# Optimization experiments

Measured on AMD Instinct MI355X. Metric: run time of the kernel, lower is better.

The kernel has to match this reference:

```python
import jax, jax.numpy as jnp
import numpy as np

OBS_LEN = 20
K = 20          # number of latent samples (leading dim of pred_lstm_hidden)
B = 4096        # batch
C = 2           # n_coordinates
H = 128         # z_dim + s_dim
MH = 64         # mapping hidden dim


def hardsigmoid(x):
    return jnp.clip(x / 6.0 + 0.5, 0.0, 1.0)


def hardtanh(x):
    return jnp.clip(x, -1.0, 1.0)


def setup_inputs() -> dict:
    key = jax.random.key(0)
    ks = jax.random.split(key, 12)
    std = 0.1  # _initialize_weights: normal(0, 0.1), biases zero
    return {
        "obs_traj_rel": jax.random.normal(ks[0], (OBS_LEN, B, C), jnp.float32),
        "pred_lstm_hidden": jax.random.normal(ks[1], (K, B, H), jnp.float32),
        # mapping MLP: Linear(H, MH) + LeakyReLU, Linear(MH, H)
        "Wm1": std * jax.random.normal(ks[2], (MH, H), jnp.float32),
        "bm1": jnp.zeros((MH,), jnp.float32),
        "Wm2": std * jax.random.normal(ks[3], (H, MH), jnp.float32),
        "bm2": jnp.zeros((H,), jnp.float32),
        # custom LSTMCell params
        "W_ih": std * jax.random.normal(ks[4], (4 * H, C), jnp.float32),
        "W_hh": std * jax.random.normal(ks[5], (4 * H, H), jnp.float32),
        "b_ih": jnp.zeros((4 * H,), jnp.float32),
        "b_hh": jnp.zeros((4 * H,), jnp.float32),
        # pred_hidden2pos: Linear(H, C)
        "W_out": std * jax.random.normal(ks[6], (C, H), jnp.float32),
        "b_out": jnp.zeros((C,), jnp.float32),
    }


def reference(obs_traj_rel, pred_lstm_hidden, Wm1, bm1, Wm2, bm2,
              W_ih, W_hh, b_ih, b_hh, W_out, b_out):
    # mapping MLP over last dim: [K, B, H]
    h = jax.nn.leaky_relu(jnp.einsum('kbh,mh->kbm', pred_lstm_hidden, Wm1) + bm1)
    h = jnp.einsum('kbm,hm->kbh', h, Wm2) + bm2
    c = jnp.zeros_like(h)

    # step i uses obs_traj_rel[max(i-1, 0)]
    idx = np.concatenate([[0], np.arange(OBS_LEN - 1)])
    inputs_seq = obs_traj_rel[idx, :, :C]  # [T, B, C]

    def step(carry, x_t):
        h, c = carry  # each [K, B, H]
        # input term is identical across the K samples -> compute once, broadcast
        gi = x_t @ W_ih.T + b_ih                      # [B, 4H]
        gh = jnp.einsum('kbh,gh->kbg', h, W_hh) + b_hh  # [K, B, 4H]
        gates = gi[None] + gh
        i_g, f_g, g_g, o_g = jnp.split(gates, 4, axis=-1)
        c_new = hardsigmoid(f_g) * c + hardsigmoid(i_g) * hardtanh(g_g)
        h_new = hardsigmoid(o_g) * hardtanh(c_new)
        out = jnp.einsum('kbh,ch->kbc', h_new, W_out) + b_out  # [K, B, C]
        return (h_new, c_new), out

    _, outs = jax.lax.scan(step, (h, c), inputs_seq)
    return outs  # [obs_len, K, B, C]
```

## Files before the change

kernel.cpp:

```cpp
#include <hip/hip_runtime.h>

#define NT 20
#define BT 4096
#define HD 128
#define RT 81920
#define RB 64

typedef _Float16 half8 __attribute__((ext_vector_type(8)));
typedef _Float16 half2v __attribute__((ext_vector_type(2)));
typedef float f32x4 __attribute__((ext_vector_type(4)));
typedef float f32x2 __attribute__((ext_vector_type(2)));
typedef unsigned u32x4 __attribute__((ext_vector_type(4)));

#if defined(__has_builtin)
#  if __has_builtin(__builtin_amdgcn_fdot2)
#    define HAVE_FDOT2 1
#  endif
#endif

__device__ __forceinline__ float clamp01(float x) {
  return fminf(fmaxf(x, 0.0f), 1.0f);
}
__device__ __forceinline__ float htanh(float x) {
  return fminf(fmaxf(x, -1.0f), 1.0f);
}

__device__ __forceinline__ float dot2(half2v a, half2v b, float c) {
#ifdef HAVE_FDOT2
  return __builtin_amdgcn_fdot2(a, b, c, false);
#else
  return fmaf((float)a[0], (float)b[0], fmaf((float)a[1], (float)b[1], c));
#endif
}

__device__ __forceinline__ half8 ldcvt8s(const float* __restrict__ p, float s) {
  f32x4 a = *(const f32x4*)p;
  f32x4 b = *(const f32x4*)(p + 4);
  half8 r;
  r[0] = (_Float16)(a[0] * s); r[1] = (_Float16)(a[1] * s);
  r[2] = (_Float16)(a[2] * s); r[3] = (_Float16)(a[3] * s);
  r[4] = (_Float16)(b[0] * s); r[5] = (_Float16)(b[1] * s);
  r[6] = (_Float16)(b[2] * s); r[7] = (_Float16)(b[3] * s);
  return r;
}
__device__ __forceinline__ half8 ldcvt8(const float* __restrict__ p) {
  return ldcvt8s(p, 1.0f);
}

__device__ __forceinline__ void lds_barrier() {
  __builtin_amdgcn_sched_barrier(0);
  asm volatile("s_waitcnt lgkmcnt(0)" ::: "memory");
  __builtin_amdgcn_s_barrier();
  __builtin_amdgcn_sched_barrier(0);
}

__global__ __launch_bounds__(512, 2) void decoder_kernel(
    const float* __restrict__ obs, const float* __restrict__ pred,
    const float* __restrict__ Wm1, const float* __restrict__ bm1,
    const float* __restrict__ Wm2, const float* __restrict__ bm2,
    const float* __restrict__ W_ih, const float* __restrict__ W_hh,
    const float* __restrict__ b_ih, const float* __restrict__ b_hh,
    const float* __restrict__ W_out, const float* __restrict__ b_out,
    float* __restrict__ outp)
{
  __shared__ __align__(16) char lds[38400];
  const int tid = threadIdx.x;
  const int w   = tid >> 6;
  const int l   = tid & 63;
  const int l15 = l & 15;
  const int lg  = l >> 4;
  const int wm  = w & 3;
  const int wc  = w >> 2;
  const int r0  = blockIdx.x * RB;
  const int b0  = r0 & (BT - 1);

  char* const buf0 = lds;
  char* const h1l  = lds + 16384;
  char* const obsl = lds + 32768;
  char* const wol  = lds + 37888;

  const f32x4 fzero = {0.f, 0.f, 0.f, 0.f};
  const float SCL = 1.0f / 6.0f;

  const int rdmask = (l15 & 7) << 4;
  const int arow  = l15 * 256;
  const int base0 = (16 * lg) ^ rdmask;
  const int wcol2 = 32 * w + 2 * l15;

  int wbase[4];
#pragma unroll
  for (int reg = 0; reg < 4; ++reg) {
    int rr = 4 * lg + reg;
    wbase[reg] = rr * 256 + (wcol2 ^ ((rr & 7) << 4));
  }

  if (tid < 256) ((_Float16*)wol)[tid] = (_Float16)W_out[tid];
  for (int i = tid; i < NT * RB; i += 512) {
    int t = i >> 6, row = i & 63;
    int tp = (t > 0) ? t - 1 : 0;
    f32x2 xv = *(const f32x2*)(obs + ((size_t)tp * BT + b0 + row) * 2);
    half2v hp; hp[0] = (_Float16)xv[0]; hp[1] = (_Float16)xv[1];
    *(unsigned*)(obsl + (size_t)i * 4) = __builtin_bit_cast(unsigned, hp);
  }

  {
    half8 a1[4], b1[2][4];
#pragma unroll
    for (int kt = 0; kt < 4; ++kt)
      a1[kt] = ldcvt8(pred + (size_t)(r0 + 16 * wm + l15) * HD + kt * 32 + lg * 8);
#pragma unroll
    for (int j = 0; j < 2; ++j)
#pragma unroll
      for (int kt = 0; kt < 4; ++kt)
        b1[j][kt] = ldcvt8(Wm1 + (l15 + 16 * (2 * wc + j)) * HD + kt * 32 + lg * 8);
    f32x4 acc1[2] = {fzero, fzero};
#pragma unroll
    for (int kt = 0; kt < 4; ++kt)
#pragma unroll
      for (int j = 0; j < 2; ++j)
        acc1[j] = __builtin_amdgcn_mfma_f32_16x16x32_f16(a1[kt], b1[j][kt], acc1[j], 0, 0, 0);
#pragma unroll
    for (int j = 0; j < 2; ++j) {
      int c = l15 + 16 * (2 * wc + j);
      float bb = bm1[c];
#pragma unroll
      for (int reg = 0; reg < 4; ++reg) {
        int row = 16 * wm + 4 * lg + reg;
        float v = acc1[j][reg] + bb;
        v = v >= 0.f ? v : 0.01f * v;
        *(_Float16*)(h1l + row * 128 + ((2 * c) ^ ((row & 7) << 4))) = (_Float16)v;
      }
    }
  }
  __syncthreads();
  {
    half8 a2[2], b2[4][2];
#pragma unroll
    for (int kt = 0; kt < 2; ++kt)
      a2[kt] = *(const half8*)(h1l + (16 * wm + l15) * 128 + ((64 * kt + 16 * lg) ^ rdmask));
#pragma unroll
    for (int j = 0; j < 4; ++j)
#pragma unroll
      for (int kt = 0; kt < 2; ++kt)
        b2[j][kt] = ldcvt8(Wm2 + (l15 + 16 * (4 * wc + j)) * 64 + kt * 32 + lg * 8);
    f32x4 acc2[4] = {fzero, fzero, fzero, fzero};
#pragma unroll
    for (int kt = 0; kt < 2; ++kt)
#pragma unroll
      for (int j = 0; j < 4; ++j)
        acc2[j] = __builtin_amdgcn_mfma_f32_16x16x32_f16(a2[kt], b2[j][kt], acc2[j], 0, 0, 0);
#pragma unroll
    for (int j = 0; j < 4; ++j) {
      int c = l15 + 16 * (4 * wc + j);
      float bb = bm2[c];
#pragma unroll
      for (int reg = 0; reg < 4; ++reg) {
        int row = 16 * wm + 4 * lg + reg;
        float v = acc2[j][reg] + bb;
        *(_Float16*)(buf0 + row * 256 + ((2 * c) ^ ((row & 7) << 4))) = (_Float16)v;
      }
    }
  }

  half8 bW[4][4];
  half8 bAug[4];
#pragma unroll
  for (int n = 0; n < 4; ++n) {
    const float s = (n == 2) ? 1.0f : SCL;
    int g = 128 * n + 16 * w + l15;
#pragma unroll
    for (int kt = 0; kt < 4; ++kt)
      bW[n][kt] = ldcvt8s(W_hh + (size_t)g * HD + kt * 32 + lg * 8, s);
    half2v t2;
    t2[0] = (_Float16)(W_ih[g * 2 + 0] * s);
    t2[1] = (_Float16)(W_ih[g * 2 + 1] * s);
    float bs = b_ih[g] + b_hh[g];
    half2v t3;
    t3[0] = (_Float16)((n == 2) ? bs : bs * SCL + 0.5f);
    t3[1] = (_Float16)0.0f;
    unsigned v0 = (lg == 0) ? __builtin_bit_cast(unsigned, t2) : 0u;
    unsigned v1 = (lg == 0) ? __builtin_bit_cast(unsigned, t3) : 0u;
    u32x4 bu = {v0, v1, 0u, 0u};
    bAug[n] = __builtin_bit_cast(half8, bu);
  }
  const float bo = wc ? b_out[1] : b_out[0];

  f32x4 cst[4] = {fzero, fzero, fzero, fzero};

  __syncthreads();

  half8 wfr[4];
#pragma unroll
  for (int kt = 0; kt < 4; ++kt)
    wfr[kt] = *(const half8*)(wol + wc * 256 + kt * 64 + lg * 16);

  for (int t = 0; t < NT; ++t) {
    char* const brd = lds + ((t & 1) << 14);
    char* const bwr = lds + (((t & 1) ^ 1) << 14);

    half8 A[2][5];

    {
      const int mm0 = (wm + 1) & 3;
#pragma unroll
      for (int kt = 0; kt < 4; ++kt)
        A[0][kt] = *(const half8*)(brd + mm0 * 4096 + arow + ((64 * kt) ^ base0));
      unsigned xv = *(const unsigned*)(obsl + ((t << 6) + (mm0 << 4) + l15) * 4);
      unsigned u0 = (lg == 0) ? xv : 0u;
      unsigned u1 = (lg == 0) ? 0x00003C00u : 0u;
      u32x4 xu = {u0, u1, 0u, 0u};
      A[0][4] = __builtin_bit_cast(half8, xu);
    }

#pragma unroll
    for (int j = 0; j < 4; ++j) {
      const int mm = (wm + 1 + j) & 3;
      const int cur = j & 1;

      if (j < 3) {
        const int mn = (wm + 2 + j) & 3;
#pragma unroll
        for (int kt = 0; kt < 4; ++kt)
          A[cur ^ 1][kt] = *(const half8*)(brd + mn * 4096 + arow + ((64 * kt) ^ base0));
        unsigned xv = *(const unsigned*)(obsl + ((t << 6) + (mn << 4) + l15) * 4);
        unsigned u0 = (lg == 0) ? xv : 0u;
        unsigned u1 = (lg == 0) ? 0x00003C00u : 0u;
        u32x4 xu = {u0, u1, 0u, 0u};
        A[cur ^ 1][4] = __builtin_bit_cast(half8, xu);
      }

      f32x4 acc[4] = {fzero, fzero, fzero, fzero};
      __builtin_amdgcn_s_setprio(1);
#pragma unroll
      for (int kt = 0; kt < 5; ++kt) {
#pragma unroll
        for (int n = 0; n < 4; ++n) {
          const half8 bfrag = (kt < 4) ? bW[n][kt] : bAug[n];
          acc[n] = __builtin_amdgcn_mfma_f32_16x16x32_f16(A[cur][kt], bfrag, acc[n], 0, 0, 0);
        }
      }
      __builtin_amdgcn_s_setprio(0);

      if (j == 3 && t > 0) {
        float p = 0.f;
#pragma unroll
        for (int kt = 0; kt < 4; ++kt) {
          const half8 a = A[cur][kt];
          const half8 wf = wfr[kt];
#pragma unroll
          for (int pp = 0; pp < 4; ++pp) {
            half2v ha; ha[0] = a[2 * pp]; ha[1] = a[2 * pp + 1];
            half2v wa; wa[0] = wf[2 * pp]; wa[1] = wf[2 * pp + 1];
            p = dot2(ha, wa, p);
          }
        }
        p += __shfl_xor(p, 16, 64); p += __shfl_xor(p, 32, 64);
        if (l < 16)
          outp[(size_t)(t - 1) * (RT * 2) + (size_t)(r0 + 16 * wm + l) * 2 + wc] = p + bo;
      }

      f32x4 cn4;
#pragma unroll
      for (int reg = 0; reg < 4; ++reg) {
        float i_ = clamp01(acc[0][reg]);
        float f_ = clamp01(acc[1][reg]);
        float g_ = htanh(acc[2][reg]);
        float o_ = clamp01(acc[3][reg]);
        float cn = fmaf(f_, cst[j][reg], i_ * g_);
        cn4[reg] = cn;
        float hn = o_ * htanh(cn);
        *(_Float16*)(bwr + mm * 4096 + wbase[reg]) = (_Float16)hn;
      }
      cst[j] = cn4;
    }
    lds_barrier();
  }

  {
    float p = 0.f;
#pragma unroll
    for (int kt = 0; kt < 4; ++kt) {
      half8 a = *(const half8*)(buf0 + wm * 4096 + arow + ((64 * kt) ^ base0));
      const half8 wf = wfr[kt];
#pragma unroll
      for (int pp = 0; pp < 4; ++pp) {
        half2v ha; ha[0] = a[2 * pp]; ha[1] = a[2 * pp + 1];
        half2v wa; wa[0] = wf[2 * pp]; wa[1] = wf[2 * pp + 1];
        p = dot2(ha, wa, p);
      }
    }
    p += __shfl_xor(p, 16, 64); p += __shfl_xor(p, 32, 64);
    if (l < 16)
      outp[(size_t)19 * (RT * 2) + (size_t)(r0 + 16 * wm + l) * 2 + wc] = p + bo;
  }
}

extern "C" void kernel_launch(void* const* d_in, const int* in_sizes, int n_in,
                              void* d_out, int out_size, void* d_ws, size_t ws_size,
                              hipStream_t stream) {
  const float* obs   = (const float*)d_in[0];
  const float* pred  = (const float*)d_in[1];
  const float* Wm1   = (const float*)d_in[2];
  const float* bm1   = (const float*)d_in[3];
  const float* Wm2   = (const float*)d_in[4];
  const float* bm2   = (const float*)d_in[5];
  const float* W_ih  = (const float*)d_in[6];
  const float* W_hh  = (const float*)d_in[7];
  const float* b_ih  = (const float*)d_in[8];
  const float* b_hh  = (const float*)d_in[9];
  const float* W_out = (const float*)d_in[10];
  const float* b_out = (const float*)d_in[11];

  decoder_kernel<<<RT / RB, 512, 0, stream>>>(
      obs, pred, Wm1, bm1, Wm2, bm2, W_ih, W_hh, b_ih, b_hh, W_out, b_out,
      (float*)d_out);
}
```

Baseline: 303.9 us.

## Process 128 rows per block, interleaving two independent row halves per wave

Result: slower. 318.6 us (+4.9%).

```diff
diff --git a/kernel.cpp b/kernel.cpp
--- a/kernel.cpp
+++ b/kernel.cpp
@@ -4,7 +4,7 @@
 #define BT 4096
 #define HD 128
 #define RT 81920
-#define RB 64
+#define RB 128
 
 typedef _Float16 half8 __attribute__((ext_vector_type(8)));
 typedef _Float16 half2v __attribute__((ext_vector_type(2)));
@@ -63,7 +63,7 @@
     const float* __restrict__ W_out, const float* __restrict__ b_out,
     float* __restrict__ outp)
 {
-  __shared__ __align__(16) char lds[38400];
+  __shared__ __align__(16) char lds[76288];
   const int tid = threadIdx.x;
   const int w   = tid >> 6;
   const int l   = tid & 63;
@@ -75,9 +75,9 @@
   const int b0  = r0 & (BT - 1);
 
   char* const buf0 = lds;
-  char* const h1l  = lds + 16384;
-  char* const obsl = lds + 32768;
-  char* const wol  = lds + 37888;
+  char* const h1l  = lds + 32768;
+  char* const obsl = lds + 65536;
+  char* const wol  = lds + 75776;
 
   const f32x4 fzero = {0.f, 0.f, 0.f, 0.f};
   const float SCL = 1.0f / 6.0f;
@@ -96,7 +96,7 @@
 
   if (tid < 256) ((_Float16*)wol)[tid] = (_Float16)W_out[tid];
   for (int i = tid; i < NT * RB; i += 512) {
-    int t = i >> 6, row = i & 63;
+    int t = i >> 7, row = i & 127;
     int tp = (t > 0) ? t - 1 : 0;
     f32x2 xv = *(const f32x2*)(obs + ((size_t)tp * BT + b0 + row) * 2);
     half2v hp; hp[0] = (_Float16)xv[0]; hp[1] = (_Float16)xv[1];
@@ -104,62 +104,80 @@
   }
 
   {
-    half8 a1[4], b1[2][4];
-#pragma unroll
-    for (int kt = 0; kt < 4; ++kt)
-      a1[kt] = ldcvt8(pred + (size_t)(r0 + 16 * wm + l15) * HD + kt * 32 + lg * 8);
+    half8 a1[2][4], b1[2][4];
+#pragma unroll
+    for (int h = 0; h < 2; ++h)
+#pragma unroll
+      for (int kt = 0; kt < 4; ++kt)
+        a1[h][kt] = ldcvt8(pred + (size_t)(r0 + 64 * h + 16 * wm + l15) * HD + kt * 32 + lg * 8);
 #pragma unroll
     for (int j = 0; j < 2; ++j)
 #pragma unroll
       for (int kt = 0; kt < 4; ++kt)
         b1[j][kt] = ldcvt8(Wm1 + (l15 + 16 * (2 * wc + j)) * HD + kt * 32 + lg * 8);
-    f32x4 acc1[2] = {fzero, fzero};
+    f32x4 acc1[2][2] = {{fzero, fzero}, {fzero, fzero}};
 #pragma unroll
     for (int kt = 0; kt < 4; ++kt)
 #pragma unroll
-      for (int j = 0; j < 2; ++j)
-        acc1[j] = __builtin_amdgcn_mfma_f32_16x16x32_f16(a1[kt], b1[j][kt], acc1[j], 0, 0, 0);
-#pragma unroll
-    for (int j = 0; j < 2; ++j) {
-      int c = l15 + 16 * (2 * wc + j);
-      float bb = bm1[c];
-#pragma unroll
-      for (int reg = 0; reg < 4; ++reg) {
-        int row = 16 * wm + 4 * lg + reg;
-        float v = acc1[j][reg] + bb;
-        v = v >= 0.f ? v : 0.01f * v;
-        *(_Float16*)(h1l + row * 128 + ((2 * c) ^ ((row & 7) << 4))) = (_Float16)v;
-      }
-    }
+      for (int h = 0; h < 2; ++h)
+#pragma unroll
+        for (int j = 0; j < 2; ++j)
+          acc1[h][j] = __builtin_amdgcn_mfma_f32_16x16x32_f16(a1[h][kt], b1[j][kt], acc1[h][j], 0, 0, 0);
+#pragma unroll
+    for (int h = 0; h < 2; ++h)
+#pragma unroll
+      for (int j = 0; j < 2; ++j) {
+        int c = l15 + 16 * (2 * wc + j);
+        float bb = bm1[c];
+#pragma unroll
+        for (int reg = 0; reg < 4; ++reg) {
+          int row = 64 * h + 16 * wm + 4 * lg + reg;
+          float v = acc1[h][j][reg] + bb;
+          v = v >= 0.f ? v : 0.01f * v;
+          *(_Float16*)(h1l + row * 128 + ((2 * c) ^ ((row & 7) << 4))) = (_Float16)v;
+        }
+      }
   }
   __syncthreads();
   {
-    half8 a2[2], b2[4][2];
-#pragma unroll
-    for (int kt = 0; kt < 2; ++kt)
-      a2[kt] = *(const half8*)(h1l + (16 * wm + l15) * 128 + ((64 * kt + 16 * lg) ^ rdmask));
+    half8 a2[2][2], b2[4][2];
+#pragma unroll
+    for (int h = 0; h < 2; ++h)
+#pragma unroll
+      for (int kt = 0; kt < 2; ++kt) {
+        int row = 64 * h + 16 * wm + l15;
+        a2[h][kt] = *(const half8*)(h1l + row * 128 + ((64 * kt + 16 * lg) ^ rdmask));
+      }
 #pragma unroll
     for (int j = 0; j < 4; ++j)
 #pragma unroll
       for (int kt = 0; kt < 2; ++kt)
         b2[j][kt] = ldcvt8(Wm2 + (l15 + 16 * (4 * wc + j)) * 64 + kt * 32 + lg * 8);
-    f32x4 acc2[4] = {fzero, fzero, fzero, fzero};
+    f32x4 acc2[2][4];
+#pragma unroll
+    for (int h = 0; h < 2; ++h)
+#pragma unroll
+      for (int j = 0; j < 4; ++j) acc2[h][j] = fzero;
 #pragma unroll
     for (int kt = 0; kt < 2; ++kt)
 #pragma unroll
-      for (int j = 0; j < 4; ++j)
-        acc2[j] = __builtin_amdgcn_mfma_f32_16x16x32_f16(a2[kt], b2[j][kt], acc2[j], 0, 0, 0);
-#pragma unroll
-    for (int j = 0; j < 4; ++j) {
-      int c = l15 + 16 * (4 * wc + j);
-      float bb = bm2[c];
-#pragma unroll
-      for (int reg = 0; reg < 4; ++reg) {
-        int row = 16 * wm + 4 * lg + reg;
-        float v = acc2[j][reg] + bb;
-        *(_Float16*)(buf0 + row * 256 + ((2 * c) ^ ((row & 7) << 4))) = (_Float16)v;
-      }
-    }
+      for (int h = 0; h < 2; ++h)
+#pragma unroll
+        for (int j = 0; j < 4; ++j)
+          acc2[h][j] = __builtin_amdgcn_mfma_f32_16x16x32_f16(a2[h][kt], b2[j][kt], acc2[h][j], 0, 0, 0);
+#pragma unroll
+    for (int h = 0; h < 2; ++h)
+#pragma unroll
+      for (int j = 0; j < 4; ++j) {
+        int c = l15 + 16 * (4 * wc + j);
+        float bb = bm2[c];
+#pragma unroll
+        for (int reg = 0; reg < 4; ++reg) {
+          int row = 64 * h + 16 * wm + 4 * lg + reg;
+          float v = acc2[h][j][reg] + bb;
+          *(_Float16*)(buf0 + row * 256 + ((2 * c) ^ ((row & 7) << 4))) = (_Float16)v;
+        }
+      }
   }
 
   half8 bW[4][4];
@@ -185,113 +203,120 @@
   }
   const float bo = wc ? b_out[1] : b_out[0];
 
-  f32x4 cst[4] = {fzero, fzero, fzero, fzero};
+  f32x4 cst[2][4];
+#pragma unroll
+  for (int h = 0; h < 2; ++h)
+#pragma unroll
+    for (int j = 0; j < 4; ++j) cst[h][j] = fzero;
 
   __syncthreads();
 
-  half8 wfr[4];
-#pragma unroll
-  for (int kt = 0; kt < 4; ++kt)
-    wfr[kt] = *(const half8*)(wol + wc * 256 + kt * 64 + lg * 16);
-
   for (int t = 0; t < NT; ++t) {
-    char* const brd = lds + ((t & 1) << 14);
-    char* const bwr = lds + (((t & 1) ^ 1) << 14);
-
-    half8 A[2][5];
-
-    {
-      const int mm0 = (wm + 1) & 3;
-#pragma unroll
-      for (int kt = 0; kt < 4; ++kt)
-        A[0][kt] = *(const half8*)(brd + mm0 * 4096 + arow + ((64 * kt) ^ base0));
-      unsigned xv = *(const unsigned*)(obsl + ((t << 6) + (mm0 << 4) + l15) * 4);
-      unsigned u0 = (lg == 0) ? xv : 0u;
-      unsigned u1 = (lg == 0) ? 0x00003C00u : 0u;
-      u32x4 xu = {u0, u1, 0u, 0u};
-      A[0][4] = __builtin_bit_cast(half8, xu);
-    }
+    char* const brd = lds + ((t & 1) << 15);
+    char* const bwr = lds + (((t & 1) ^ 1) << 15);
 
 #pragma unroll
     for (int j = 0; j < 4; ++j) {
       const int mm = (wm + 1 + j) & 3;
-      const int cur = j & 1;
-
-      if (j < 3) {
-        const int mn = (wm + 2 + j) & 3;
-#pragma unroll
-        for (int kt = 0; kt < 4; ++kt)
-          A[cur ^ 1][kt] = *(const half8*)(brd + mn * 4096 + arow + ((64 * kt) ^ base0));
-        unsigned xv = *(const unsigned*)(obsl + ((t << 6) + (mn << 4) + l15) * 4);
-        unsigned u0 = (lg == 0) ? xv : 0u;
-        unsigned u1 = (lg == 0) ? 0x00003C00u : 0u;
-        u32x4 xu = {u0, u1, 0u, 0u};
-        A[cur ^ 1][4] = __builtin_bit_cast(half8, xu);
-      }
-
-      f32x4 acc[4] = {fzero, fzero, fzero, fzero};
+
+      half8 A0[5], A1[5];
+#pragma unroll
+      for (int kt = 0; kt < 4; ++kt) {
+        A0[kt] = *(const half8*)(brd + mm * 4096 + arow + ((64 * kt) ^ base0));
+        A1[kt] = *(const half8*)(brd + (mm + 4) * 4096 + arow + ((64 * kt) ^ base0));
+      }
+      {
+        unsigned xv0 = *(const unsigned*)(obsl + ((t << 7) + (mm << 4) + l15) * 4);
+        unsigned xv1 = *(const unsigned*)(obsl + ((t << 7) + ((mm + 4) << 4) + l15) * 4);
+        unsigned u1c = (lg == 0) ? 0x00003C00u : 0u;
+        u32x4 xu0 = {(lg == 0) ? xv0 : 0u, u1c, 0u, 0u};
+        u32x4 xu1 = {(lg == 0) ? xv1 : 0u, u1c, 0u, 0u};
+        A0[4] = __builtin_bit_cast(half8, xu0);
+        A1[4] = __builtin_bit_cast(half8, xu1);
+      }
+
+      f32x4 acc0[4] = {fzero, fzero, fzero, fzero};
+      f32x4 acc1[4] = {fzero, fzero, fzero, fzero};
       __builtin_amdgcn_s_setprio(1);
 #pragma unroll
       for (int kt = 0; kt < 5; ++kt) {
 #pragma unroll
         for (int n = 0; n < 4; ++n) {
           const half8 bfrag = (kt < 4) ? bW[n][kt] : bAug[n];
-          acc[n] = __builtin_amdgcn_mfma_f32_16x16x32_f16(A[cur][kt], bfrag, acc[n], 0, 0, 0);
+          acc0[n] = __builtin_amdgcn_mfma_f32_16x16x32_f16(A0[kt], bfrag, acc0[n], 0, 0, 0);
+          acc1[n] = __builtin_amdgcn_mfma_f32_16x16x32_f16(A1[kt], bfrag, acc1[n], 0, 0, 0);
         }
       }
       __builtin_amdgcn_s_setprio(0);
 
       if (j == 3 && t > 0) {
-        float p = 0.f;
+        float p0 = 0.f, p1 = 0.f;
 #pragma unroll
         for (int kt = 0; kt < 4; ++kt) {
-          const half8 a = A[cur][kt];
-          const half8 wf = wfr[kt];
+          const half8 wf = *(const half8*)(wol + wc * 256 + kt * 64 + lg * 16);
+          const half8 a0 = A0[kt], a1 = A1[kt];
 #pragma unroll
           for (int pp = 0; pp < 4; ++pp) {
-            half2v ha; ha[0] = a[2 * pp]; ha[1] = a[2 * pp + 1];
             half2v wa; wa[0] = wf[2 * pp]; wa[1] = wf[2 * pp + 1];
-            p = dot2(ha, wa, p);
+            half2v h0; h0[0] = a0[2 * pp]; h0[1] = a0[2 * pp + 1];
+            half2v h1; h1[0] = a1[2 * pp]; h1[1] = a1[2 * pp + 1];
+            p0 = dot2(h0, wa, p0);
+            p1 = dot2(h1, wa, p1);
           }
         }
-        p += __shfl_xor(p, 16, 64); p += __shfl_xor(p, 32, 64);
-        if (l < 16)
-          outp[(size_t)(t - 1) * (RT * 2) + (size_t)(r0 + 16 * wm + l) * 2 + wc] = p + bo;
-      }
-
-      f32x4 cn4;
-#pragma unroll
-      for (int reg = 0; reg < 4; ++reg) {
-        float i_ = clamp01(acc[0][reg]);
-        float f_ = clamp01(acc[1][reg]);
-        float g_ = htanh(acc[2][reg]);
-        float o_ = clamp01(acc[3][reg]);
-        float cn = fmaf(f_, cst[j][reg], i_ * g_);
-        cn4[reg] = cn;
-        float hn = o_ * htanh(cn);
-        *(_Float16*)(bwr + mm * 4096 + wbase[reg]) = (_Float16)hn;
-      }
-      cst[j] = cn4;
+        p0 += __shfl_xor(p0, 16, 64); p0 += __shfl_xor(p0, 32, 64);
+        p1 += __shfl_xor(p1, 16, 64); p1 += __shfl_xor(p1, 32, 64);
+        if (l < 16) {
+          size_t base = (size_t)(t - 1) * (RT * 2);
+          outp[base + (size_t)(r0 + 16 * wm + l) * 2 + wc] = p0 + bo;
+          outp[base + (size_t)(r0 + 64 + 16 * wm + l) * 2 + wc] = p1 + bo;
+        }
+      }
+
+#pragma unroll
+      for (int h = 0; h < 2; ++h) {
+        const f32x4* ac = h ? acc1 : acc0;
+        f32x4 cn4;
+#pragma unroll
+        for (int reg = 0; reg < 4; ++reg) {
+          float i_ = clamp01(ac[0][reg]);
+          float f_ = clamp01(ac[1][reg]);
+          float g_ = htanh(ac[2][reg]);
+          float o_ = clamp01(ac[3][reg]);
+          float cn = fmaf(f_, cst[h][j][reg], i_ * g_);
+          cn4[reg] = cn;
+          float hn = o_ * htanh(cn);
+          *(_Float16*)(bwr + (mm + 4 * h) * 4096 + wbase[reg]) = (_Float16)hn;
+        }
+        cst[h][j] = cn4;
+      }
     }
     lds_barrier();
   }
 
   {
-    float p = 0.f;
+    float p0 = 0.f, p1 = 0.f;
 #pragma unroll
     for (int kt = 0; kt < 4; ++kt) {
-      half8 a = *(const half8*)(buf0 + wm * 4096 + arow + ((64 * kt) ^ base0));
-      const half8 wf = wfr[kt];
+      const half8 wf = *(const half8*)(wol + wc * 256 + kt * 64 + lg * 16);
+      half8 a0 = *(const half8*)(buf0 + wm * 4096 + arow + ((64 * kt) ^ base0));
+      half8 a1 = *(const half8*)(buf0 + (wm + 4) * 4096 + arow + ((64 * kt) ^ base0));
 #pragma unroll
       for (int pp = 0; pp < 4; ++pp) {
-        half2v ha; ha[0] = a[2 * pp]; ha[1] = a[2 * pp + 1];
         half2v wa; wa[0] = wf[2 * pp]; wa[1] = wf[2 * pp + 1];
-        p = dot2(ha, wa, p);
+        half2v h0; h0[0] = a0[2 * pp]; h0[1] = a0[2 * pp + 1];
+        half2v h1; h1[0] = a1[2 * pp]; h1[1] = a1[2 * pp + 1];
+        p0 = dot2(h0, wa, p0);
+        p1 = dot2(h1, wa, p1);
       }
     }
-    p += __shfl_xor(p, 16, 64); p += __shfl_xor(p, 32, 64);
-    if (l < 16)
-      outp[(size_t)19 * (RT * 2) + (size_t)(r0 + 16 * wm + l) * 2 + wc] = p + bo;
+    p0 += __shfl_xor(p0, 16, 64); p0 += __shfl_xor(p0, 32, 64);
+    p1 += __shfl_xor(p1, 16, 64); p1 += __shfl_xor(p1, 32, 64);
+    if (l < 16) {
+      size_t base = (size_t)19 * (RT * 2);
+      outp[base + (size_t)(r0 + 16 * wm + l) * 2 + wc] = p0 + bo;
+      outp[base + (size_t)(r0 + 64 + 16 * wm + l) * 2 + wc] = p1 + bo;
+    }
   }
 }
 
```
